# Optimization experiments

Hardware: AMD Instinct MI355X
Metric: run time of the kernel (lower is better)

## Reference

```python
import jax, jax.numpy as jnp
import numpy as np

N = 16384  # n_nodes
D = 64     # feature dim


def setup_inputs() -> dict:
    key = jax.random.key(0)
    kx, ka = jax.random.split(key)
    x = jax.random.normal(kx, (N, D), dtype=jnp.float32)
    # original code only tests adj[idx] == 1, so 0/1 int entries are faithful
    adj = jax.random.randint(ka, (N, N), 0, 2, dtype=jnp.int32)
    return {"x": x, "adj": adj}


def reference(x, adj):
    # GraphPool: for each node, sum its own feature vector plus the feature
    # vectors of all neighbors j with adj[i, j] == 1.
    # Vectorized: out = adj @ x + x  (dense binary SpMM + self term).
    a = (adj == 1).astype(x.dtype)  # [N, N]
    return jnp.matmul(a, x) + x     # [N, D]
```

## Files before the change

kernel.cpp:

```cpp
#include <hip/hip_runtime.h>

#define NN 16384
#define DD 64

typedef _Float16 f16x8 __attribute__((ext_vector_type(8)));
typedef short    s16x8 __attribute__((ext_vector_type(8)));
typedef float    f32x4 __attribute__((ext_vector_type(4)));
typedef int      i32x4 __attribute__((ext_vector_type(4)));

__global__ __launch_bounds__(256) void prep_x(const float* __restrict__ x,
                                              _Float16* __restrict__ ws) {
    int tid = blockIdx.x * 256 + threadIdx.x;
    int l  = tid & 63;
    int tc = tid >> 6;
    int c  = tc & 3;
    int t  = tc >> 2;
    int q  = l >> 4;
    int m  = l & 15;
    int row0 = t * 32 + q * 8;
    int col  = c * 16 + m;
    f16x8 v;
#pragma unroll
    for (int j = 0; j < 8; ++j)
        v[j] = (_Float16)x[(size_t)(row0 + j) * DD + col];
    *(f16x8*)(ws + (size_t)tid * 8) = v;
}

__global__ __launch_bounds__(256) void graphpool_gemm(const int* __restrict__ adj,
                                                      const float* __restrict__ x,
                                                      const _Float16* __restrict__ xs,
                                                      float* __restrict__ out) {
    __shared__ _Float16 sB[2][8192];

    const int tid = threadIdx.x;
    const int w   = tid >> 6;
    const int l   = tid & 63;
    const int q   = l >> 4;
    const int m   = l & 15;
    const int row16 = blockIdx.x * 64 + w * 16;

    const int* aptr = adj + (size_t)(row16 + m) * NN + q * 8;

    f32x4 acc[4];
#pragma unroll
    for (int c = 0; c < 4; ++c) acc[c] = (f32x4){0.f, 0.f, 0.f, 0.f};

    i32x4 areg[2][4][2];
    f16x8 sreg[4];

    auto loadA = [&](int n, int buf) {
#pragma unroll
        for (int s = 0; s < 4; ++s) {
            const i32x4* p = (const i32x4*)(aptr + (size_t)n * 128 + s * 32);
            areg[buf][s][0] = __builtin_nontemporal_load(p);
            areg[buf][s][1] = __builtin_nontemporal_load(p + 1);
        }
    };
    auto stageRead = [&](int n) {
        const f16x8* src = (const f16x8*)(xs + (size_t)n * 8192);
#pragma unroll
        for (int p = 0; p < 4; ++p) sreg[p] = src[p * 256 + tid];
    };
    auto stageWrite = [&](int buf) {
        f16x8* dst = (f16x8*)sB[buf];
#pragma unroll
        for (int p = 0; p < 4; ++p) dst[p * 256 + tid] = sreg[p];
    };

    stageRead(0);
    loadA(0, 0);
    stageWrite(0);
    __syncthreads();

    auto step = [&](int n, int buf, int nb) {
        const bool pf = (n + 1 < NN / 128);
        if (pf) { stageRead(n + 1); loadA(n + 1, nb); }
#pragma unroll
        for (int s = 0; s < 4; ++s) {
            int av[8];
            {
                i32x4 v0 = areg[buf][s][0], v1 = areg[buf][s][1];
                av[0] = v0.x; av[1] = v0.y; av[2] = v0.z; av[3] = v0.w;
                av[4] = v1.x; av[5] = v1.y; av[6] = v1.z; av[7] = v1.w;
            }
            s16x8 ai;
#pragma unroll
            for (int j = 0; j < 8; ++j)
                ai[j] = av[j] ? (short)0x3C00 : (short)0;
            f16x8 af = __builtin_bit_cast(f16x8, ai);
#pragma unroll
            for (int c = 0; c < 4; ++c) {
                f16x8 bf = *(const f16x8*)&sB[buf][((s * 4 + c) * 64 + l) * 8];
                acc[c] = __builtin_amdgcn_mfma_f32_16x16x32_f16(af, bf, acc[c], 0, 0, 0);
            }
        }
        if (pf) stageWrite(nb);
        __syncthreads();
    };

    for (int n = 0; n < NN / 128; n += 2) {
        step(n,     0, 1);
        step(n + 1, 1, 0);
    }

#pragma unroll
    for (int c = 0; c < 4; ++c) {
#pragma unroll
        for (int r = 0; r < 4; ++r) {
            int row = row16 + q * 4 + r;
            int col = c * 16 + m;
            size_t off = (size_t)row * DD + col;
            out[off] = acc[c][r] + x[off];
        }
    }
}

__global__ void graphpool_fallback(const int* __restrict__ adj,
                                   const float* __restrict__ x,
                                   float* __restrict__ out) {
    int i = blockIdx.x;
    int d = threadIdx.x;
    float acc = x[(size_t)i * DD + d];
    const int* row = adj + (size_t)i * NN;
    for (int j = 0; j < NN; ++j)
        if (row[j]) acc += x[(size_t)j * DD + d];
    out[(size_t)i * DD + d] = acc;
}

extern "C" void kernel_launch(void* const* d_in, const int* in_sizes, int n_in,
                              void* d_out, int out_size, void* d_ws, size_t ws_size,
                              hipStream_t stream) {
    const float* x   = (const float*)d_in[0];
    const int*   adj = (const int*)d_in[1];
    float*       out = (float*)d_out;

    const size_t ws_needed = (size_t)NN * DD * sizeof(_Float16);
    if (ws_size >= ws_needed) {
        _Float16* xs = (_Float16*)d_ws;
        prep_x<<<512, 256, 0, stream>>>(x, xs);
        graphpool_gemm<<<NN / 64, 256, 0, stream>>>(adj, x, xs, out);
    } else {
        graphpool_fallback<<<NN, 64, 0, stream>>>(adj, x, out);
    }
}
```

Before: 1.388 ms.

## Replace shared-memory B staging with per-wave register loads and single-wave blocks

Each block becomes one wavefront computing 16 rows, loading the fp16 x tiles directly from global memory into a double-buffered register array instead of staging through LDS. This removes the __syncthreads barriers and LDS writes/reads per step, letting waves progress independently. The cost is four times more global/L2 reads of the B operand and higher register pressure, which may lower occupancy.

New measurement: 1.417 ms. +2.1%, slower.

```diff
diff --git a/kernel.cpp b/kernel.cpp
--- a/kernel.cpp
+++ b/kernel.cpp
@@ -26,55 +26,40 @@
     *(f16x8*)(ws + (size_t)tid * 8) = v;
 }
 
-__global__ __launch_bounds__(256) void graphpool_gemm(const int* __restrict__ adj,
-                                                      const float* __restrict__ x,
-                                                      const _Float16* __restrict__ xs,
-                                                      float* __restrict__ out) {
-    __shared__ _Float16 sB[2][8192];
-
-    const int tid = threadIdx.x;
-    const int w   = tid >> 6;
-    const int l   = tid & 63;
-    const int q   = l >> 4;
-    const int m   = l & 15;
-    const int row16 = blockIdx.x * 64 + w * 16;
+__global__ __launch_bounds__(64, 2) void graphpool_gemm(const int* __restrict__ adj,
+                                                        const float* __restrict__ x,
+                                                        const _Float16* __restrict__ xs,
+                                                        float* __restrict__ out) {
+    const int l = threadIdx.x;
+    const int q = l >> 4;
+    const int m = l & 15;
+    const int row16 = blockIdx.x * 16;
 
     const int* aptr = adj + (size_t)(row16 + m) * NN + q * 8;
+    const f16x8* bbase = (const f16x8*)xs + l;
 
     f32x4 acc[4];
 #pragma unroll
     for (int c = 0; c < 4; ++c) acc[c] = (f32x4){0.f, 0.f, 0.f, 0.f};
 
     i32x4 areg[2][4][2];
-    f16x8 sreg[4];
+    f16x8 breg[2][16];
 
     auto loadA = [&](int n, int buf) {
+        const int* base = aptr + (size_t)n * 128;
 #pragma unroll
         for (int s = 0; s < 4; ++s) {
-            const i32x4* p = (const i32x4*)(aptr + (size_t)n * 128 + s * 32);
+            const i32x4* p = (const i32x4*)(base + s * 32);
             areg[buf][s][0] = __builtin_nontemporal_load(p);
             areg[buf][s][1] = __builtin_nontemporal_load(p + 1);
         }
     };
-    auto stageRead = [&](int n) {
-        const f16x8* src = (const f16x8*)(xs + (size_t)n * 8192);
+    auto loadB = [&](int n, int buf) {
+        const f16x8* src = bbase + (size_t)n * 1024;
 #pragma unroll
-        for (int p = 0; p < 4; ++p) sreg[p] = src[p * 256 + tid];
+        for (int f = 0; f < 16; ++f) breg[buf][f] = src[f * 64];
     };
-    auto stageWrite = [&](int buf) {
-        f16x8* dst = (f16x8*)sB[buf];
-#pragma unroll
-        for (int p = 0; p < 4; ++p) dst[p * 256 + tid] = sreg[p];
-    };
-
-    stageRead(0);
-    loadA(0, 0);
-    stageWrite(0);
-    __syncthreads();
-
-    auto step = [&](int n, int buf, int nb) {
-        const bool pf = (n + 1 < NN / 128);
-        if (pf) { stageRead(n + 1); loadA(n + 1, nb); }
+    auto compute = [&](int buf) {
 #pragma unroll
         for (int s = 0; s < 4; ++s) {
             int av[8];
@@ -89,18 +74,20 @@
                 ai[j] = av[j] ? (short)0x3C00 : (short)0;
             f16x8 af = __builtin_bit_cast(f16x8, ai);
 #pragma unroll
-            for (int c = 0; c < 4; ++c) {
-                f16x8 bf = *(const f16x8*)&sB[buf][((s * 4 + c) * 64 + l) * 8];
-                acc[c] = __builtin_amdgcn_mfma_f32_16x16x32_f16(af, bf, acc[c], 0, 0, 0);
-            }
+            for (int c = 0; c < 4; ++c)
+                acc[c] = __builtin_amdgcn_mfma_f32_16x16x32_f16(af, breg[buf][s * 4 + c],
+                                                                acc[c], 0, 0, 0);
         }
-        if (pf) stageWrite(nb);
-        __syncthreads();
     };
 
+    loadB(0, 0);
+    loadA(0, 0);
+
     for (int n = 0; n < NN / 128; n += 2) {
-        step(n,     0, 1);
-        step(n + 1, 1, 0);
+        if (n + 1 < NN / 128) { loadB(n + 1, 1); loadA(n + 1, 1); }
+        compute(0);
+        if (n + 2 < NN / 128) { loadB(n + 2, 0); loadA(n + 2, 0); }
+        compute(1);
     }
 
 #pragma unroll
@@ -138,7 +125,7 @@
     if (ws_size >= ws_needed) {
         _Float16* xs = (_Float16*)d_ws;
         prep_x<<<512, 256, 0, stream>>>(x, xs);
-        graphpool_gemm<<<NN / 64, 256, 0, stream>>>(adj, x, xs, out);
+        graphpool_gemm<<<NN / 16, 64, 0, stream>>>(adj, x, xs, out);
     } else {
         graphpool_fallback<<<NN, 64, 0, stream>>>(adj, x, out);
     }
```
